# Optimization experiments

Measured on AMD Instinct MI355X. Metric: run time of the kernel, lower is better.

Reference implementation:

```python
import jax, jax.numpy as jnp
import numpy as np

N_NODES = 100000   # n_entities + n_users
N_REL = 16
N_EDGES = 1600000
D = 64             # entity_dim == relation_dim
DIMS = [64, 32, 16, 16, 8]
NEG_SLOPE = 0.01   # nn.LeakyReLU default
EPS = 1e-12        # F.normalize default eps


def setup_inputs() -> dict:
    key = jax.random.key(0)
    ks = jax.random.split(key, 16)
    def lin(k, i, o):
        return jax.random.normal(k, (i, o), jnp.float32) / np.sqrt(i)
    inp = {
        'emb': jax.random.normal(ks[0], (N_NODES, D), jnp.float32) * 0.1,
        'rel_embed': jax.random.normal(ks[1], (N_REL, D), jnp.float32) * 0.1,
        'W_R': jax.random.normal(ks[2], (N_REL, D, D), jnp.float32) / np.sqrt(D),
        'W0': lin(ks[3], DIMS[0], DIMS[1]), 'b0': jnp.zeros((DIMS[1],), jnp.float32),
        'W1': lin(ks[4], DIMS[1], DIMS[2]), 'b1': jnp.zeros((DIMS[2],), jnp.float32),
        'W2': lin(ks[5], DIMS[2], DIMS[3]), 'b2': jnp.zeros((DIMS[3],), jnp.float32),
        'W3': lin(ks[6], DIMS[3], DIMS[4]), 'b3': jnp.zeros((DIMS[4],), jnp.float32),
        'src': jax.random.randint(ks[7], (N_EDGES,), 0, N_NODES, jnp.int32),
        'dst': jnp.sort(jax.random.randint(ks[8], (N_EDGES,), 0, N_NODES, jnp.int32)),
        'etype': jax.random.randint(ks[9], (N_EDGES,), 0, N_REL, jnp.int32),
    }
    return inp


def _lrelu(x):
    return jnp.where(x >= 0, x, NEG_SLOPE * x)


def _l2norm(x):
    n = jnp.sqrt(jnp.sum(x * x, axis=1, keepdims=True))
    return x / jnp.maximum(n, EPS)


def reference(emb, rel_embed, W_R, W0, b0, W1, b1, W2, b2, W3, b3, src, dst, etype):
    N = emb.shape[0]
    # --- compute_attention: TransR-style per-edge score (vectorized over relations) ---
    # all_mul[n, r, :] = emb[n] @ W_R[r]  (equivalent to the per-relation loop)
    all_mul = jnp.einsum('nd,rdk->nrk', emb, W_R)          # (N, R, D)
    r_mul_t = all_mul[src, etype]                          # edges.src transformed (E, D)
    r_mul_h = all_mul[dst, etype]                          # edges.dst transformed (E, D)
    att = jnp.sum(r_mul_t * jnp.tanh(r_mul_h + rel_embed[etype]), axis=-1)  # (E,)
    # --- edge softmax grouped by destination node ---
    m = jax.ops.segment_max(att, dst, num_segments=N)
    e = jnp.exp(att - m[dst])
    s = jax.ops.segment_sum(e, dst, num_segments=N)
    att = (e / s[dst])[:, None]                            # (E, 1)

    Ws = [(W0, b0), (W1, b1), (W2, b2), (W3, b3)]
    results = []
    for index in range(1, 5):
        ego = emb
        all_embed = [ego]
        for i, (W, b) in enumerate(Ws):
            if i < index:
                # u_mul_e('node','att') + sum over incoming edges
                N_h = jax.ops.segment_sum(att * ego[src], dst, num_segments=N)
                ego = _lrelu((ego + N_h) @ W + b)          # gcn aggregator, type 0
            else:
                ego = _lrelu(ego @ W + b)                  # type 1: linear only
            all_embed.append(_l2norm(ego))
        results.append(jnp.concatenate(all_embed, axis=1))  # (N, 136)
    return jnp.stack(results)                               # (4, N, 136)
```

## Files before the change

kernel.cpp:

```cpp
#include <hip/hip_runtime.h>
#include <hip/hip_bf16.h>
#include <math.h>

#define N_NODES 100000
#define N_RELS 16
#define N_EDGES 1600000
#define OUTW 136
#define NEG_SLOPE 0.01f
#define RES ((size_t)N_NODES * OUTW)

typedef __attribute__((ext_vector_type(8))) short short8;
typedef __attribute__((ext_vector_type(4))) float f32x4;

__device__ __forceinline__ float lrelu(float x) { return x >= 0.f ? x : NEG_SLOPE * x; }
__device__ __forceinline__ float fast_rcp(float x) { return __builtin_amdgcn_rcpf(x); }
__device__ __forceinline__ float fast_tanh(float x) {
    float e = __expf(2.f * x);
    return 1.f - 2.f * fast_rcp(e + 1.f);
}
__device__ __forceinline__ unsigned short f2bf(float f) {
    union { float f; unsigned u; } v; v.f = f;
    unsigned x = v.u + 0x7FFF + ((v.u >> 16) & 1);
    return (unsigned short)(x >> 16);
}

__global__ __launch_bounds__(256) void k_prep(const float* __restrict__ emb, unsigned short* __restrict__ embB,
                                              const float* __restrict__ WR, unsigned short* __restrict__ WT,
                                              const float* __restrict__ W0, const float* __restrict__ W1,
                                              const float* __restrict__ W2, const float* __restrict__ W3,
                                              float* __restrict__ WLT,
                                              const int* __restrict__ dst, int* __restrict__ offs,
                                              int* __restrict__ cnt) {
    int blk = blockIdx.x, tid = threadIdx.x;
    if (blk < 6250) {
        int id = blk * 256 + tid;
        float4 v = *(const float4*)(emb + (size_t)id * 4);
        ushort4 o; o.x = f2bf(v.x); o.y = f2bf(v.y); o.z = f2bf(v.z); o.w = f2bf(v.w);
        *(ushort4*)(embB + (size_t)id * 4) = o;
    } else if (blk < 6506) {
        int id = (blk - 6250) * 256 + tid;
        int r = id >> 12, rem = id & 4095, n = rem >> 6, k = rem & 63;
        WT[id] = f2bf(WR[(r << 12) + (k << 6) + n]);
    } else if (blk < 6518) {
        int id = (blk - 6506) * 256 + tid;
        if (id < 2944) {
            float v;
            if (id < 2048)      { int c = id >> 6, k = id & 63;                  v = W0[k * 32 + c]; }
            else if (id < 2560) { int r = id - 2048; int c = r >> 5, k = r & 31; v = W1[k * 16 + c]; }
            else if (id < 2816) { int r = id - 2560; int c = r >> 4, k = r & 15; v = W2[k * 16 + c]; }
            else                { int r = id - 2816; int c = r >> 4, k = r & 15; v = W3[k * 8 + c]; }
            WLT[id] = v;
        }
    } else if (blk < 6909) {
        int n = (blk - 6518) * 256 + tid;
        if (n <= N_NODES) {
            int lo = 0, hi = N_EDGES;
            while (lo < hi) { int mid = (lo + hi) >> 1; if (dst[mid] < n) lo = mid + 1; else hi = mid; }
            offs[n] = lo;
        }
    } else {
        if (tid < 16) cnt[tid] = 0;
    }
}

__global__ __launch_bounds__(256) void k_hist(const int* __restrict__ etype, int* __restrict__ cnt) {
    __shared__ int lcnt[16];
    int tid = threadIdx.x;
    if (tid < 16) lcnt[tid] = 0;
    __syncthreads();
    atomicAdd(&lcnt[etype[blockIdx.x * 256 + tid]], 1);
    __syncthreads();
    if (tid < 16 && lcnt[tid]) atomicAdd(&cnt[tid], lcnt[tid]);
}

__global__ void k_scan(const int* __restrict__ cnt, int* __restrict__ roff, int* __restrict__ cur,
                       int* __restrict__ bo) {
    if (threadIdx.x == 0) {
        int a = 0, nb = 0;
        for (int r = 0; r < 16; ++r) {
            roff[r] = a; cur[r] = a; bo[r] = nb;
            a += cnt[r]; nb += (cnt[r] + 15) >> 4;
        }
        roff[16] = a; bo[16] = nb;
    }
}

__global__ __launch_bounds__(256) void k_scatter(const int* __restrict__ etype,
                                                 const int* __restrict__ src,
                                                 const int* __restrict__ dst,
                                                 int* __restrict__ cur, int* __restrict__ eperm,
                                                 int* __restrict__ srcp, int* __restrict__ dstp) {
    __shared__ int lcnt[16], lbase[16], loff[16];
    int tid = threadIdx.x;
    if (tid < 16) { lcnt[tid] = 0; loff[tid] = 0; }
    __syncthreads();
    int e = blockIdx.x * 256 + tid;
    int t = etype[e];
    atomicAdd(&lcnt[t], 1);
    __syncthreads();
    if (tid < 16) lbase[tid] = lcnt[tid] ? atomicAdd(&cur[tid], lcnt[tid]) : 0;
    __syncthreads();
    int rank = atomicAdd(&loff[t], 1);
    int pos = lbase[t] + rank;
    eperm[pos] = e;
    srcp[pos] = src[e];
    dstp[pos] = dst[e];
}

__global__ __launch_bounds__(256) void k_edge_attF(const unsigned short* __restrict__ embB,
                                                   const unsigned short* __restrict__ WT,
                                                   const float* __restrict__ rel,
                                                   const int* __restrict__ srcp,
                                                   const int* __restrict__ dstp,
                                                   const int* __restrict__ eperm,
                                                   const int* __restrict__ roff,
                                                   const int* __restrict__ bo,
                                                   float* __restrict__ att) {
    __shared__ int sro[17], sbo[17];
    int tid = threadIdx.x;
    if (tid < 17) { sro[tid] = roff[tid]; sbo[tid] = bo[tid]; }
    __syncthreads();
    int w = tid >> 6, l = tid & 63;
    int rlo = l & 15, rhi = l >> 4;
    int gw = blockIdx.x * 4 + w;
    int nw = gridDim.x * 4;
    int NB = sbo[16];
    int per = (NB + nw - 1) / nw;
    int start = gw * per;
    int end = start + per < NB ? start + per : NB;
    if (start >= end) return;

    int r = 0;
    while (sbo[r + 1] <= start) ++r;

    short8 bfr[4][2];
    float relv[4];
    {
        const unsigned short* wt = WT + ((size_t)r << 12);
        #pragma unroll
        for (int cb = 0; cb < 4; ++cb) {
            bfr[cb][0] = *(const short8*)(wt + (cb * 16 + rlo) * 64 + rhi * 8);
            bfr[cb][1] = *(const short8*)(wt + (cb * 16 + rlo) * 64 + 32 + rhi * 8);
            relv[cb] = rel[r * 64 + cb * 16 + rlo];
        }
    }

    for (int g = start; g < end; ++g) {
        if (g >= sbo[r + 1]) {
            while (sbo[r + 1] <= g) ++r;
            const unsigned short* wt = WT + ((size_t)r << 12);
            #pragma unroll
            for (int cb = 0; cb < 4; ++cb) {
                bfr[cb][0] = *(const short8*)(wt + (cb * 16 + rlo) * 64 + rhi * 8);
                bfr[cb][1] = *(const short8*)(wt + (cb * 16 + rlo) * 64 + 32 + rhi * 8);
                relv[cb] = rel[r * 64 + cb * 16 + rlo];
            }
        }
        int i0 = sro[r] + (g - sbo[r]) * 16;
        int hi = sro[r + 1];
        int ea = i0 + rlo; if (ea >= hi) ea = hi - 1;
        size_t sA = (size_t)srcp[ea], sB = (size_t)dstp[ea];
        short8 at0 = *(const short8*)(embB + sA * 64 + rhi * 8);
        short8 at1 = *(const short8*)(embB + sA * 64 + 32 + rhi * 8);
        short8 ah0 = *(const short8*)(embB + sB * 64 + rhi * 8);
        short8 ah1 = *(const short8*)(embB + sB * 64 + 32 + rhi * 8);
        f32x4 accT[4], accH[4];
        #pragma unroll
        for (int cb = 0; cb < 4; ++cb) {
            accT[cb] = (f32x4){0.f, 0.f, 0.f, 0.f};
            accH[cb] = (f32x4){0.f, 0.f, 0.f, 0.f};
            accT[cb] = __builtin_amdgcn_mfma_f32_16x16x32_bf16(at0, bfr[cb][0], accT[cb], 0, 0, 0);
            accT[cb] = __builtin_amdgcn_mfma_f32_16x16x32_bf16(at1, bfr[cb][1], accT[cb], 0, 0, 0);
            accH[cb] = __builtin_amdgcn_mfma_f32_16x16x32_bf16(ah0, bfr[cb][0], accH[cb], 0, 0, 0);
            accH[cb] = __builtin_amdgcn_mfma_f32_16x16x32_bf16(ah1, bfr[cb][1], accH[cb], 0, 0, 0);
        }
        #pragma unroll
        for (int i = 0; i < 4; ++i) {
            float s = 0.f;
            #pragma unroll
            for (int cb = 0; cb < 4; ++cb)
                s += accT[cb][i] * fast_tanh(accH[cb][i] + relv[cb]);
            s += __shfl_xor(s, 1); s += __shfl_xor(s, 2);
            s += __shfl_xor(s, 4); s += __shfl_xor(s, 8);
            int idx = i0 + rhi * 4 + i;
            if (rlo == 0 && idx < hi) att[eperm[idx]] = s;
        }
    }
}

__global__ __launch_bounds__(256) void k_softmax(float* __restrict__ att, const int* __restrict__ offs) {
    int tid = threadIdx.x;
    int n = blockIdx.x * 32 + (tid >> 3);
    int j = tid & 7;
    int b = offs[n], e = offs[n + 1];
    if (b >= e) return;
    float m = -INFINITY;
    for (int i = b + j; i < e; i += 8) m = fmaxf(m, att[i]);
    #pragma unroll
    for (int s = 4; s >= 1; s >>= 1) m = fmaxf(m, __shfl_xor(m, s));
    float sum = 0.f;
    for (int i = b + j; i < e; i += 8) { float v = __expf(att[i] - m); att[i] = v; sum += v; }
    #pragma unroll
    for (int s = 4; s >= 1; s >>= 1) sum += __shfl_xor(sum, s);
    float inv = fast_rcp(sum);
    for (int i = b + j; i < e; i += 8) att[i] *= inv;
}

__global__ __launch_bounds__(256) void k_dense0(const float* __restrict__ emb,
                                                const float* __restrict__ WLT,
                                                float* __restrict__ Y0,
                                                float* __restrict__ out) {
    int tid = threadIdx.x, w = tid >> 6, l = tid & 63;
    int c = l & 31, g = l >> 5;
    float Wreg[32];
    #pragma unroll
    for (int kk = 0; kk < 32; ++kk) Wreg[kk] = WLT[(size_t)c * 64 + g * 32 + kk];
    int nw = gridDim.x * 4;
    for (int n = blockIdx.x * 4 + w; n < N_NODES; n += nw) {
        const float* xr = emb + (size_t)n * 64;
        float v = xr[l];
        #pragma unroll
        for (int r = 0; r < 4; ++r)
            out[(size_t)r * RES + (size_t)n * OUTW + l] = v;
        float o = 0.f;
        #pragma unroll
        for (int kk = 0; kk < 32; kk += 4) {
            float4 xv = *(const float4*)(xr + g * 32 + kk);
            o += xv.x * Wreg[kk] + xv.y * Wreg[kk + 1] + xv.z * Wreg[kk + 2] + xv.w * Wreg[kk + 3];
        }
        o += __shfl_xor(o, 32);
        if (l < 32) Y0[(size_t)n * 32 + c] = o;
    }
}

template<int D, int DN, int COL, int RSTART, bool PROJ>
__global__ __launch_bounds__(256) void k_aggF(const float* __restrict__ Y,
                                              const float* __restrict__ att,
                                              const int* __restrict__ src,
                                              const int* __restrict__ offs,
                                              const float* __restrict__ bias,
                                              const float* __restrict__ WTn,
                                              float* __restrict__ Yn,
                                              float* __restrict__ out) {
    constexpr int E = D / 4;
    constexpr int S = 64 / E;
    constexpr int G = PROJ ? (64 / DN) : 1;
    constexpr int KS = PROJ ? (D / G) : 1;
    __shared__ float xm[4][PROJ ? D : 4];
    int tid = threadIdx.x, w = tid >> 6, l = tid & 63;
    int n = blockIdx.x * 4 + w;
    int b = offs[n], e = offs[n + 1];
    int je = l & (E - 1), slot = l / E;

    float Wreg[KS];
    if constexpr (PROJ) {
        int c = l & (DN - 1), g = l / DN;
        #pragma unroll
        for (int kk = 0; kk < KS; ++kk) Wreg[kk] = WTn[(size_t)c * D + g * KS + kk];
    }

    float4 a = make_float4(0.f, 0.f, 0.f, 0.f);
    int i = b + slot;
    for (; i + S < e; i += 2 * S) {
        float t0 = att[i], t1 = att[i + S];
        float4 p0 = *(const float4*)(Y + (size_t)src[i]     * D + 4 * je);
        float4 p1 = *(const float4*)(Y + (size_t)src[i + S] * D + 4 * je);
        a.x += t0 * p0.x + t1 * p1.x;
        a.y += t0 * p0.y + t1 * p1.y;
        a.z += t0 * p0.z + t1 * p1.z;
        a.w += t0 * p0.w + t1 * p1.w;
    }
    for (; i < e; i += S) {
        float t0 = att[i];
        float4 p0 = *(const float4*)(Y + (size_t)src[i] * D + 4 * je);
        a.x += t0 * p0.x; a.y += t0 * p0.y; a.z += t0 * p0.z; a.w += t0 * p0.w;
    }
    #pragma unroll
    for (int st = E; st < 64; st <<= 1) {
        a.x += __shfl_xor(a.x, st); a.y += __shfl_xor(a.y, st);
        a.z += __shfl_xor(a.z, st); a.w += __shfl_xor(a.w, st);
    }
    float4 q  = *(const float4*)(Y + (size_t)n * D + 4 * je);
    float4 bi = *(const float4*)(bias + 4 * je);
    float4 u;
    u.x = lrelu(a.x + q.x + bi.x);
    u.y = lrelu(a.y + q.y + bi.y);
    u.z = lrelu(a.z + q.z + bi.z);
    u.w = lrelu(a.w + q.w + bi.w);
    float ss = u.x * u.x + u.y * u.y + u.z * u.z + u.w * u.w;
    #pragma unroll
    for (int st = 1; st < E; st <<= 1) ss += __shfl_xor(ss, st);
    float inv = fast_rcp(fmaxf(sqrtf(ss), 1e-12f));
    if (slot < 4 - RSTART) {
        float4 nr = make_float4(u.x * inv, u.y * inv, u.z * inv, u.w * inv);
        *(float4*)(out + (size_t)(RSTART + slot) * RES + (size_t)n * OUTW + COL + 4 * je) = nr;
    }
    if constexpr (PROJ) {
        if (slot == S - 1) *(float4*)&xm[w][4 * je] = u;
        __builtin_amdgcn_s_waitcnt(0);
        __builtin_amdgcn_sched_barrier(0);
        int c = l & (DN - 1), g = l / DN;
        float o = 0.f;
        if constexpr (KS >= 4) {
            #pragma unroll
            for (int kk = 0; kk < KS; kk += 4) {
                float4 xv = *(const float4*)&xm[w][g * KS + kk];
                o += xv.x * Wreg[kk] + xv.y * Wreg[kk + 1] + xv.z * Wreg[kk + 2] + xv.w * Wreg[kk + 3];
            }
        } else {
            float2 xv = *(const float2*)&xm[w][g * KS];
            o += xv.x * Wreg[0] + xv.y * Wreg[1];
        }
        #pragma unroll
        for (int st = DN; st < 64; st <<= 1) o += __shfl_xor(o, st);
        if (l < DN) Yn[(size_t)n * DN + c] = o;
    }
}

__global__ __launch_bounds__(256) void k_bchain(const float* __restrict__ Y1,
                                                const float* __restrict__ Y2,
                                                const float* __restrict__ Y3,
                                                const float* __restrict__ WLT,
                                                const float* __restrict__ b1,
                                                const float* __restrict__ b2,
                                                const float* __restrict__ b3,
                                                float* __restrict__ out) {
    __shared__ float W2s[16][17], W3s[8][17];
    __shared__ float bb1[16], bb2[16], bb3[8];
    __shared__ float mid[16][17], mid2[16][17];
    int tid = threadIdx.x;
    if (tid < 256) W2s[tid >> 4][tid & 15] = WLT[2560 + tid];
    if (tid < 128) W3s[tid >> 4][tid & 15] = WLT[2816 + tid];
    if (tid < 16) bb1[tid] = b1[tid];
    if (tid >= 32 && tid < 48) bb2[tid - 32] = b2[tid - 32];
    if (tid >= 64 && tid < 72) bb3[tid - 64] = b3[tid - 64];
    __syncthreads();

    int grp = tid >> 4, lj = tid & 15;
    int seg = blockIdx.x / 6250;
    int nb = blockIdx.x % 6250;
    int n = nb * 16 + grp;

    if (seg == 0) {
        float u1 = lrelu(Y1[(size_t)n * 16 + lj] + bb1[lj]);
        mid[grp][lj] = u1;
        float ss = u1 * u1;
        #pragma unroll
        for (int m = 8; m >= 1; m >>= 1) ss += __shfl_xor(ss, m);
        out[(size_t)n * OUTW + 96 + lj] = u1 * fast_rcp(fmaxf(sqrtf(ss), 1e-12f));
        __builtin_amdgcn_s_waitcnt(0);
        __builtin_amdgcn_sched_barrier(0);
        float o2 = bb2[lj];
        #pragma unroll
        for (int k = 0; k < 16; ++k) o2 += mid[grp][k] * W2s[lj][k];
        float u2 = lrelu(o2);
        mid2[grp][lj] = u2;
        float s2 = u2 * u2;
        #pragma unroll
        for (int m = 8; m >= 1; m >>= 1) s2 += __shfl_xor(s2, m);
        out[(size_t)n * OUTW + 112 + lj] = u2 * fast_rcp(fmaxf(sqrtf(s2), 1e-12f));
        __builtin_amdgcn_s_waitcnt(0);
        __builtin_amdgcn_sched_barrier(0);
        if (lj < 8) {
            float o3 = bb3[lj];
            #pragma unroll
            for (int k = 0; k < 16; ++k) o3 += mid2[grp][k] * W3s[lj][k];
            float u3 = lrelu(o3);
            float s3 = u3 * u3;
            #pragma unroll
            for (int m = 4; m >= 1; m >>= 1) s3 += __shfl_xor(s3, m);
            out[(size_t)n * OUTW + 128 + lj] = u3 * fast_rcp(fmaxf(sqrtf(s3), 1e-12f));
        }
    } else if (seg == 1) {
        float u2 = lrelu(Y2[(size_t)n * 16 + lj] + bb2[lj]);
        mid[grp][lj] = u2;
        float s2 = u2 * u2;
        #pragma unroll
        for (int m = 8; m >= 1; m >>= 1) s2 += __shfl_xor(s2, m);
        out[RES + (size_t)n * OUTW + 112 + lj] = u2 * fast_rcp(fmaxf(sqrtf(s2), 1e-12f));
        __builtin_amdgcn_s_waitcnt(0);
        __builtin_amdgcn_sched_barrier(0);
        if (lj < 8) {
            float o3 = bb3[lj];
            #pragma unroll
            for (int k = 0; k < 16; ++k) o3 += mid[grp][k] * W3s[lj][k];
            float u3 = lrelu(o3);
            float s3 = u3 * u3;
            #pragma unroll
            for (int m = 4; m >= 1; m >>= 1) s3 += __shfl_xor(s3, m);
            out[RES + (size_t)n * OUTW + 128 + lj] = u3 * fast_rcp(fmaxf(sqrtf(s3), 1e-12f));
        }
    } else {
        if (lj < 8) {
            float u3 = lrelu(Y3[(size_t)n * 8 + lj] + bb3[lj]);
            float s3 = u3 * u3;
            #pragma unroll
            for (int m = 4; m >= 1; m >>= 1) s3 += __shfl_xor(s3, m);
            out[2 * RES + (size_t)n * OUTW + 128 + lj] = u3 * fast_rcp(fmaxf(sqrtf(s3), 1e-12f));
        }
    }
}

extern "C" void kernel_launch(void* const* d_in, const int* in_sizes, int n_in,
                              void* d_out, int out_size, void* d_ws, size_t ws_size,
                              hipStream_t stream) {
    (void)in_sizes; (void)n_in; (void)out_size; (void)ws_size;
    const float* emb = (const float*)d_in[0];
    const float* rel_embed = (const float*)d_in[1];
    const float* W_R = (const float*)d_in[2];
    const float* W0 = (const float*)d_in[3];  const float* b0 = (const float*)d_in[4];
    const float* W1 = (const float*)d_in[5];  const float* b1 = (const float*)d_in[6];
    const float* W2 = (const float*)d_in[7];  const float* b2 = (const float*)d_in[8];
    const float* W3 = (const float*)d_in[9];  const float* b3 = (const float*)d_in[10];
    const int* src = (const int*)d_in[11];
    const int* dst = (const int*)d_in[12];
    const int* etype = (const int*)d_in[13];
    float* out = (float*)d_out;

    char* p = (char*)d_ws;
    auto alloc = [&](size_t bytes) { char* q = p; p += (bytes + 255) & ~(size_t)255; return q; };
    int* offs  = (int*)alloc((size_t)(N_NODES + 1) * 4);
    float* att = (float*)alloc((size_t)N_EDGES * 4);
    int* eperm = (int*)alloc((size_t)N_EDGES * 4);
    int* srcp  = (int*)alloc((size_t)N_EDGES * 4);
    int* dstp  = (int*)alloc((size_t)N_EDGES * 4);
    int* cnt   = (int*)alloc(64);
    int* roff  = (int*)alloc(68);
    int* cur   = (int*)alloc(64);
    int* bo    = (int*)alloc(68);
    unsigned short* embB = (unsigned short*)alloc((size_t)N_NODES * 64 * 2);
    unsigned short* WT   = (unsigned short*)alloc((size_t)65536 * 2);
    float* WLT = (float*)alloc((size_t)2944 * 4);
    float* Y0  = (float*)alloc((size_t)N_NODES * 32 * 4);
    float* Y1  = (float*)alloc((size_t)N_NODES * 16 * 4);
    float* Y2  = (float*)alloc((size_t)N_NODES * 16 * 4);
    float* Y3  = (float*)alloc((size_t)N_NODES * 8 * 4);

    k_prep<<<6910, 256, 0, stream>>>(emb, embB, W_R, WT, W0, W1, W2, W3, WLT, dst, offs, cnt);
    k_hist<<<N_EDGES / 256, 256, 0, stream>>>(etype, cnt);
    k_scan<<<1, 64, 0, stream>>>(cnt, roff, cur, bo);
    k_scatter<<<N_EDGES / 256, 256, 0, stream>>>(etype, src, dst, cur, eperm, srcp, dstp);

    k_edge_attF<<<2048, 256, 0, stream>>>(embB, WT, rel_embed, srcp, dstp, eperm, roff, bo, att);
    k_softmax<<<N_NODES / 32, 256, 0, stream>>>(att, offs);

    k_dense0<<<3125, 256, 0, stream>>>(emb, WLT, Y0, out);

    k_aggF<32, 16,  64, 0, true ><<<N_NODES / 4, 256, 0, stream>>>(Y0, att, src, offs, b0, WLT + 2048, Y1, out);
    k_aggF<16, 16,  96, 1, true ><<<N_NODES / 4, 256, 0, stream>>>(Y1, att, src, offs, b1, WLT + 2560, Y2, out);
    k_aggF<16,  8, 112, 2, true ><<<N_NODES / 4, 256, 0, stream>>>(Y2, att, src, offs, b2, WLT + 2816, Y3, out);
    k_aggF< 8,  8, 128, 3, false><<<N_NODES / 4, 256, 0, stream>>>(Y3, att, src, offs, b3, nullptr, nullptr, out);

    k_bchain<<<18750, 256, 0, stream>>>(Y1, Y2, Y3, WLT, b1, b2, b3, out);
}
```

Measured before the change: 554.5 us.

## Assign edge-attention blocks per relation and software-prefetch next edge gathers

The edge attention kernel now gives each relation a fixed 128 blocks, so a block loads that relation's weights once and walks its 16-edge groups with a grid stride. The block-offset table and its scan output are removed. Each iteration prefetches the embedding rows for the next group and the indices for the group after that, so gather latency overlaps the MFMA and tanh work. The fixed split can leave load imbalance if relation counts differ, and the extra prefetch registers may lower occupancy.

```diff
diff --git a/kernel.cpp b/kernel.cpp
--- a/kernel.cpp
+++ b/kernel.cpp
@@ -73,15 +73,11 @@
     if (tid < 16 && lcnt[tid]) atomicAdd(&cnt[tid], lcnt[tid]);
 }
 
-__global__ void k_scan(const int* __restrict__ cnt, int* __restrict__ roff, int* __restrict__ cur,
-                       int* __restrict__ bo) {
+__global__ void k_scan(const int* __restrict__ cnt, int* __restrict__ roff, int* __restrict__ cur) {
     if (threadIdx.x == 0) {
-        int a = 0, nb = 0;
-        for (int r = 0; r < 16; ++r) {
-            roff[r] = a; cur[r] = a; bo[r] = nb;
-            a += cnt[r]; nb += (cnt[r] + 15) >> 4;
-        }
-        roff[16] = a; bo[16] = nb;
+        int a = 0;
+        for (int r = 0; r < 16; ++r) { roff[r] = a; cur[r] = a; a += cnt[r]; }
+        roff[16] = a;
     }
 }
 
@@ -114,56 +110,54 @@
                                                    const int* __restrict__ dstp,
                                                    const int* __restrict__ eperm,
                                                    const int* __restrict__ roff,
-                                                   const int* __restrict__ bo,
                                                    float* __restrict__ att) {
-    __shared__ int sro[17], sbo[17];
-    int tid = threadIdx.x;
-    if (tid < 17) { sro[tid] = roff[tid]; sbo[tid] = bo[tid]; }
-    __syncthreads();
-    int w = tid >> 6, l = tid & 63;
+    int tid = threadIdx.x, w = tid >> 6, l = tid & 63;
     int rlo = l & 15, rhi = l >> 4;
-    int gw = blockIdx.x * 4 + w;
-    int nw = gridDim.x * 4;
-    int NB = sbo[16];
-    int per = (NB + nw - 1) / nw;
-    int start = gw * per;
-    int end = start + per < NB ? start + per : NB;
-    if (start >= end) return;
-
-    int r = 0;
-    while (sbo[r + 1] <= start) ++r;
-
+    int r = blockIdx.x >> 7;
+    int blk = blockIdx.x & 127;
+    int lo = roff[r], hi = roff[r + 1];
+    int nb = (hi - lo + 15) >> 4;
+    constexpr int STEP = 512;
+
+    const unsigned short* wt = WT + ((size_t)r << 12);
     short8 bfr[4][2];
     float relv[4];
-    {
-        const unsigned short* wt = WT + ((size_t)r << 12);
-        #pragma unroll
-        for (int cb = 0; cb < 4; ++cb) {
-            bfr[cb][0] = *(const short8*)(wt + (cb * 16 + rlo) * 64 + rhi * 8);
-            bfr[cb][1] = *(const short8*)(wt + (cb * 16 + rlo) * 64 + 32 + rhi * 8);
-            relv[cb] = rel[r * 64 + cb * 16 + rlo];
-        }
-    }
-
-    for (int g = start; g < end; ++g) {
-        if (g >= sbo[r + 1]) {
-            while (sbo[r + 1] <= g) ++r;
-            const unsigned short* wt = WT + ((size_t)r << 12);
-            #pragma unroll
-            for (int cb = 0; cb < 4; ++cb) {
-                bfr[cb][0] = *(const short8*)(wt + (cb * 16 + rlo) * 64 + rhi * 8);
-                bfr[cb][1] = *(const short8*)(wt + (cb * 16 + rlo) * 64 + 32 + rhi * 8);
-                relv[cb] = rel[r * 64 + cb * 16 + rlo];
-            }
-        }
-        int i0 = sro[r] + (g - sbo[r]) * 16;
-        int hi = sro[r + 1];
-        int ea = i0 + rlo; if (ea >= hi) ea = hi - 1;
-        size_t sA = (size_t)srcp[ea], sB = (size_t)dstp[ea];
-        short8 at0 = *(const short8*)(embB + sA * 64 + rhi * 8);
-        short8 at1 = *(const short8*)(embB + sA * 64 + 32 + rhi * 8);
-        short8 ah0 = *(const short8*)(embB + sB * 64 + rhi * 8);
-        short8 ah1 = *(const short8*)(embB + sB * 64 + 32 + rhi * 8);
+    #pragma unroll
+    for (int cb = 0; cb < 4; ++cb) {
+        bfr[cb][0] = *(const short8*)(wt + (cb * 16 + rlo) * 64 + rhi * 8);
+        bfr[cb][1] = *(const short8*)(wt + (cb * 16 + rlo) * 64 + 32 + rhi * 8);
+        relv[cb] = rel[r * 64 + cb * 16 + rlo];
+    }
+
+    int g0 = blk * 4 + w;
+    if (g0 >= nb) return;
+
+    auto ldidx = [&](int g, int& sa, int& sb) {
+        int ea = lo + g * 16 + rlo;
+        if (ea >= hi) ea = hi - 1;
+        sa = srcp[ea]; sb = dstp[ea];
+    };
+
+    int saC, sbC, saN, sbN;
+    ldidx(g0, saC, sbC);
+    if (g0 + STEP < nb) ldidx(g0 + STEP, saN, sbN); else { saN = saC; sbN = sbC; }
+
+    short8 at0 = *(const short8*)(embB + (size_t)saC * 64 + rhi * 8);
+    short8 at1 = *(const short8*)(embB + (size_t)saC * 64 + 32 + rhi * 8);
+    short8 ah0 = *(const short8*)(embB + (size_t)sbC * 64 + rhi * 8);
+    short8 ah1 = *(const short8*)(embB + (size_t)sbC * 64 + 32 + rhi * 8);
+
+    for (int g = g0; g < nb; g += STEP) {
+        short8 nt0, nt1, nh0, nh1;
+        bool hasn = (g + STEP) < nb;
+        if (hasn) {
+            nt0 = *(const short8*)(embB + (size_t)saN * 64 + rhi * 8);
+            nt1 = *(const short8*)(embB + (size_t)saN * 64 + 32 + rhi * 8);
+            nh0 = *(const short8*)(embB + (size_t)sbN * 64 + rhi * 8);
+            nh1 = *(const short8*)(embB + (size_t)sbN * 64 + 32 + rhi * 8);
+        }
+        if (g + 2 * STEP < nb) ldidx(g + 2 * STEP, saN, sbN);
+
         f32x4 accT[4], accH[4];
         #pragma unroll
         for (int cb = 0; cb < 4; ++cb) {
@@ -174,6 +168,7 @@
             accH[cb] = __builtin_amdgcn_mfma_f32_16x16x32_bf16(ah0, bfr[cb][0], accH[cb], 0, 0, 0);
             accH[cb] = __builtin_amdgcn_mfma_f32_16x16x32_bf16(ah1, bfr[cb][1], accH[cb], 0, 0, 0);
         }
+        int i0 = lo + g * 16;
         #pragma unroll
         for (int i = 0; i < 4; ++i) {
             float s = 0.f;
@@ -185,6 +180,7 @@
             int idx = i0 + rhi * 4 + i;
             if (rlo == 0 && idx < hi) att[eperm[idx]] = s;
         }
+        at0 = nt0; at1 = nt1; ah0 = nh0; ah1 = nh1;
     }
 }
 
@@ -427,7 +423,6 @@
     int* cnt   = (int*)alloc(64);
     int* roff  = (int*)alloc(68);
     int* cur   = (int*)alloc(64);
-    int* bo    = (int*)alloc(68);
     unsigned short* embB = (unsigned short*)alloc((size_t)N_NODES * 64 * 2);
     unsigned short* WT   = (unsigned short*)alloc((size_t)65536 * 2);
     float* WLT = (float*)alloc((size_t)2944 * 4);
@@ -438,10 +433,10 @@
 
     k_prep<<<6910, 256, 0, stream>>>(emb, embB, W_R, WT, W0, W1, W2, W3, WLT, dst, offs, cnt);
     k_hist<<<N_EDGES / 256, 256, 0, stream>>>(etype, cnt);
-    k_scan<<<1, 64, 0, stream>>>(cnt, roff, cur, bo);
+    k_scan<<<1, 64, 0, stream>>>(cnt, roff, cur);
     k_scatter<<<N_EDGES / 256, 256, 0, stream>>>(etype, src, dst, cur, eperm, srcp, dstp);
 
-    k_edge_attF<<<2048, 256, 0, stream>>>(embB, WT, rel_embed, srcp, dstp, eperm, roff, bo, att);
+    k_edge_attF<<<16 * 128, 256, 0, stream>>>(embB, WT, rel_embed, srcp, dstp, eperm, roff, att);
     k_softmax<<<N_NODES / 32, 256, 0, stream>>>(att, offs);
 
     k_dense0<<<3125, 256, 0, stream>>>(emb, WLT, Y0, out);
```

After: 527.6 us. 4.9% less time.
